# Kernel tuning notes

Measured on AMD Instinct MI355X. Metric: run time of the kernel, lower is better.

Reference implementation:

```python
import jax, jax.numpy as jnp
import numpy as np

B, T, V, D, H = 256, 64, 6207, 512, 512  # batch, seq_len, vocab, emb_dim, hidden_dim
YF = 2048   # image feature dim -> concat with h (512) = 2560 gate input
EPS = 1e-10


def setup_inputs() -> dict:
    key = jax.random.key(0)
    ks = jax.random.split(key, 20)
    # torch init_parameters(): all params ~ U(-0.05, 0.05)
    u = lambda k, s: jax.random.uniform(k, s, jnp.float32, -0.05, 0.05)
    return {
        "y": jax.random.normal(ks[0], (B, YF), jnp.float32),
        "x": jax.random.randint(ks[1], (B, T), 0, V),
        "emb_w": u(ks[2], (V, D)),
        # bottom LSTM cell (input 512 -> hidden 512), torch layout: W_ih (4H, D)
        "W_ih": u(ks[3], (4 * H, D)), "W_hh": u(ks[4], (4 * H, H)),
        "b_ih": u(ks[5], (4 * H,)), "b_hh": u(ks[6], (4 * H,)),
        # top LSTM cell (input 512 -> hidden 512)
        "W_ih_t": u(ks[7], (4 * H, H)), "W_hh_t": u(ks[8], (4 * H, H)),
        "b_ih_t": u(ks[9], (4 * H,)), "b_hh_t": u(ks[10], (4 * H,)),
        # gate linear: Linear(2560, 512)
        "Wg": u(ks[11], (H, H + YF)), "bg": u(ks[12], (H,)),
        # final linear: Linear(512, 256)
        "Wlin": u(ks[13], (256, H)), "blin": u(ks[14], (256,)),
        # per-step gumbel-sigmoid uniforms (sampled inside forward in torch;
        # precomputed here so the reference is deterministic)
        "u1": jax.random.uniform(ks[15], (T, B, H), jnp.float32),
        "u2": jax.random.uniform(ks[16], (T, B, H), jnp.float32),
    }


def _lstm_cell(xt, h, c, Wi, Wh, bi, bh):
    # torch nn.LSTM gate order: i, f, g, o
    z = xt @ Wi.T + bi + h @ Wh.T + bh          # (B, 4H)
    i, f, g, o = jnp.split(z, 4, axis=-1)
    c = jax.nn.sigmoid(f) * c + jax.nn.sigmoid(i) * jnp.tanh(g)
    h = jax.nn.sigmoid(o) * jnp.tanh(c)
    return h, c


def reference(y, x, emb_w, W_ih, W_hh, b_ih, b_hh,
              W_ih_t, W_hh_t, b_ih_t, b_hh_t, Wg, bg, Wlin, blin, u1, u2):
    xs = jnp.transpose(emb_w[x], (1, 0, 2))     # (T, B, D)

    def step(carry, ins):
        h, c, ht, ct = carry
        xt, u1t, u2t = ins
        h, c = _lstm_cell(xt, h, c, W_ih, W_hh, b_ih, b_hh)
        # gate logits: relu(Linear([h, y]))
        logits = jax.nn.relu(jnp.concatenate([h, y], axis=1) @ Wg.T + bg)
        # custom gumbel-sigmoid noise: -log(log(U2+eps)/log(U1+eps)+eps)
        noise = -jnp.log(jnp.log(u2t + EPS) / jnp.log(u1t + EPS) + EPS)
        y_soft = jax.nn.sigmoid(logits + noise)
        # hard threshold at 0.5 with straight-through estimator
        y_hard = (y_soft >= 0.5).astype(y_soft.dtype)
        gate = y_hard - jax.lax.stop_gradient(y_soft) + y_soft
        hf = h * gate
        ht, ct = _lstm_cell(hf, ht, ct, W_ih_t, W_hh_t, b_ih_t, b_hh_t)
        return (h, c, ht, ct), None

    z0 = jnp.zeros((B, H), jnp.float32)
    (_, _, ht, _), _ = jax.lax.scan(step, (z0, z0, z0, z0), (xs, u1, u2))
    # dropout is identity in eval mode; torch output is (1, B, 256), squeezed here
    return jax.nn.relu(ht @ Wlin.T + blin)      # (B, 256)
```

## Files before the change

### kernel.cpp

```cpp
#include <hip/hip_runtime.h>
#include <hip/hip_bf16.h>


typedef __attribute__((ext_vector_type(8))) short short8;
typedef __attribute__((ext_vector_type(4))) float floatx4;

#define MFMA16(a, b, c) __builtin_amdgcn_mfma_f32_16x16x32_bf16(a, b, c, 0, 0, 0)
#define AGENT __HIP_MEMORY_SCOPE_AGENT
#define HWREG_XCC_ID ((31u << 11) | (0u << 6) | 20u)

__device__ inline float bf2f(ushort u) {
    union { unsigned int u32; float f; } v; v.u32 = ((unsigned int)u) << 16; return v.f;
}
__device__ inline ushort f2bf(float f) {
    union { float f; unsigned int u; } v; v.f = f;
    return (ushort)((v.u + 0x7fffu + ((v.u >> 16) & 1u)) >> 16);
}
__device__ inline short8 ld8(const ushort* p) { return *(const short8*)p; }
__device__ inline float sigf(float x) { return 1.0f / (1.0f + expf(-x)); }
__device__ inline void mm3(floatx4& acc, short8 ah, short8 al, short8 bh, short8 bl) {
    acc = MFMA16(ah, bh, acc);
    acc = MFMA16(ah, bl, acc);
    acc = MFMA16(al, bh, acc);
}

__global__ __launch_bounds__(256) void k_prep(const float* __restrict__ w0,
                                              const float* __restrict__ w1,
                                              const float* __restrict__ w2,
                                              const float* __restrict__ w3,
                                              const float* __restrict__ wg,
                                              const float* __restrict__ wl,
                                              const float* __restrict__ em,
                                              const float* __restrict__ yy,
                                              ushort* __restrict__ wreg,
                                              uint* __restrict__ zbase) {
    unsigned i = blockIdx.x * 256u + threadIdx.x;
    if (i >= 9735712u) return;
    if (i >= 9338368u) {
        zbase[i - 9338368u] = 0u;
        return;
    }
    const float* src; ushort* hi; unsigned n, loc;
    if (i < 4194304u) {
        unsigned seg = i >> 20; loc = i & 1048575u; n = 1048576u;
        hi = wreg + seg * 2097152u;
        src = (seg == 0) ? w0 : (seg == 1) ? w1 : (seg == 2) ? w2 : w3;
    } else if (i < 5505024u) { loc = i - 4194304u; src = wg; hi = wreg + 8388608u;  n = 1310720u; }
    else if (i < 5636096u)   { loc = i - 5505024u; src = wl; hi = wreg + 11010048u; n = 131072u; }
    else if (i < 8814080u)   { loc = i - 5636096u; src = em; hi = wreg + 11272192u; n = 3177984u; }
    else                     { loc = i - 8814080u; src = yy; hi = wreg + 17628160u; n = 524288u; }
    float v = src[loc];
    ushort h = f2bf(v);
    hi[loc] = h;
    hi[n + loc] = f2bf(v - bf2f(h));
}

__global__ __launch_bounds__(512) void k_gy(const ushort* __restrict__ y_hi,
                                            const ushort* __restrict__ y_lo,
                                            const ushort* __restrict__ Wg_hi,
                                            const ushort* __restrict__ Wg_lo,
                                            const float* __restrict__ bg,
                                            float* __restrict__ gy) {
    __shared__ float zsB[4 * 528];
    int tid = threadIdx.x, lane = tid & 63, w = tid >> 6;
    int quad = lane >> 4, lr = lane & 15, q8 = quad * 8;
    int r0 = (blockIdx.x >> 4) * 16, n0 = (blockIdx.x & 15) * 32;
    int nh = w & 1, kq = w >> 1;
    int arow = r0 + lr, brow = n0 + nh * 16 + lr;
    floatx4 acc = {};
#pragma unroll
    for (int k0 = 0; k0 < 512; k0 += 32) {
        short8 ah = ld8(y_hi + arow * 2048 + kq * 512 + k0 + q8);
        short8 al = ld8(y_lo + arow * 2048 + kq * 512 + k0 + q8);
        short8 bh = ld8(Wg_hi + brow * 2560 + 512 + kq * 512 + k0 + q8);
        short8 bl = ld8(Wg_lo + brow * 2560 + 512 + kq * 512 + k0 + q8);
        mm3(acc, ah, al, bh, bl);
    }
#pragma unroll
    for (int r4 = 0; r4 < 4; r4++)
        zsB[kq * 528 + (quad * 4 + r4) * 33 + nh * 16 + lr] = acc[r4];
    __syncthreads();
    int ml = tid >> 5, jj = tid & 31;
    float s = zsB[ml * 33 + jj] + zsB[528 + ml * 33 + jj] +
              zsB[1056 + ml * 33 + jj] + zsB[1584 + ml * 33 + jj];
    gy[(r0 + ml) * 512 + n0 + jj] = s + bg[n0 + jj];
}

struct KP {
    const float *b_ih, *b_hh, *b_iht, *b_hht, *u1, *u2, *gy;
    const int* x;
    uint* gflags;
    uint* claim;
    uint *hP, *htP0, *htP1, *hfP;
    ushort *ht_hi, *ht_lo;
    const ushort *Whh_hi, *Whh_lo, *Wih_hi, *Wih_lo;
    const ushort *Wiht_hi, *Wiht_lo, *Whht_hi, *Whht_lo;
    const ushort *Wg_hi, *Wg_lo, *em_hi, *em_lo;
};

__device__ inline void gbar_arrive(uint* gf, int jb, uint g) {
    __builtin_amdgcn_s_waitcnt(0);
    asm volatile("" ::: "memory");
    __syncthreads();
    if (threadIdx.x == 0)
        __hip_atomic_store(&gf[jb], g, __ATOMIC_RELAXED, AGENT);
}
__device__ inline void gbar_wait(const uint* gf, uint g) {
    if ((threadIdx.x >> 6) == 0) {
        int l = threadIdx.x & 63;
        for (;;) {
            uint v = (l < 16) ? __hip_atomic_load(&gf[l], __ATOMIC_RELAXED, AGENT) : g;
            if (__all((int)(v >= g))) break;
            __builtin_amdgcn_s_sleep(1);
        }
    }
    __syncthreads();
}

__device__ inline void stage_state(const uint* __restrict__ src, int r0,
                                   ushort* __restrict__ dst) {
    int tid = threadIdx.x;
    int sr = tid >> 5, scol = (tid & 31) * 16;
    const unsigned long long* p =
        (const unsigned long long*)(src + (r0 + sr) * 512 + scol);
    ushort* d = dst + sr * 1032;
#pragma unroll
    for (int i = 0; i < 8; i++) {
        unsigned long long v = __hip_atomic_load(p + i, __ATOMIC_RELAXED, AGENT);
        uint u0 = (uint)v, u1v = (uint)(v >> 32);
        int c = scol + i * 2;
        *(uint*)(d + c) = (u0 & 0xffffu) | ((u1v & 0xffffu) << 16);
        *(uint*)(d + 520 + c) = (u0 >> 16) | (u1v & 0xffff0000u);
    }
}

__device__ inline void stage_emb(const ushort* __restrict__ emh,
                                 const ushort* __restrict__ eml,
                                 const int* __restrict__ x, int r0, int t,
                                 ushort* __restrict__ dst) {
    int tid = threadIdx.x;
    int sr = tid >> 5, sc = (tid & 31) * 16;
    int tok = x[(r0 + sr) * 64 + t];
    const short8* ph = (const short8*)(emh + (size_t)tok * 512 + sc);
    const short8* pl = (const short8*)(eml + (size_t)tok * 512 + sc);
    short8 h0 = ph[0], h1 = ph[1], l0 = pl[0], l1 = pl[1];
    ushort* d = dst + sr * 1032;
    *(short8*)(d + sc) = h0;       *(short8*)(d + sc + 8) = h1;
    *(short8*)(d + 520 + sc) = l0; *(short8*)(d + 520 + sc + 8) = l1;
}

__device__ inline short8 fragA(const ushort* As, int row, int k) {
    return *(const short8*)(As + row * 1032 + k);
}

__global__ void __launch_bounds__(512, 1) k_main(KP p) {
    __shared__ ushort As[16 * 1032];
    __shared__ ushort Ae[16 * 1032];
    __shared__ ushort Az[16 * 1032];
    __shared__ ushort Ac[16 * 1032];
    __shared__ float zs[16 * 132];
    __shared__ uint role_s;

    const int tid = threadIdx.x;
    const int w = tid >> 6;
    const int lane = tid & 63;
    const int quad = lane >> 4;
    const int lr = lane & 15;
    const int q8 = quad * 8;
    const float EPS = 1e-10f;

    if (tid == 0) {
        uint xcc = __builtin_amdgcn_s_getreg(HWREG_XCC_ID) & 7u;
        uint slot = __hip_atomic_fetch_add(&p.claim[xcc * 16], 1u,
                                           __ATOMIC_RELAXED, AGENT) & 31u;
        role_s = xcc * 32u + slot;
    }
    __syncthreads();
    const uint role = role_s;
    const int jb = (int)(role >> 4);
    const int g16 = (int)(role & 15u);
    const int r0 = g16 * 16, j0 = jb * 32;

    const int gate = w >> 1, nh = w & 1;
    const int brow = gate * 512 + j0 + nh * 16 + lr;
    const int kq = w >> 1;
    const int browB = j0 + nh * 16 + lr;
    const int ml = tid >> 5, jj = tid & 31;

    const float biasA = p.b_ih[brow] + p.b_hh[brow];
    const float biasC = p.b_iht[brow] + p.b_hht[brow];
    const float gy_r = p.gy[(r0 + ml) * 512 + j0 + jj];
    const ushort* WhhH = p.Whh_hi + brow * 512;
    const ushort* WhhL = p.Whh_lo + brow * 512;
    const ushort* WihH = p.Wih_hi + brow * 512;
    const ushort* WihL = p.Wih_lo + brow * 512;
    const ushort* WitH = p.Wiht_hi + brow * 512;
    const ushort* WitL = p.Wiht_lo + brow * 512;
    const ushort* WhtH = p.Whht_hi + brow * 512;
    const ushort* WhtL = p.Whht_lo + brow * 512;
    const ushort* WgH = p.Wg_hi + browB * 2560 + kq * 128;
    const ushort* WgL = p.Wg_lo + browB * 2560 + kq * 128;
    const float* pu1 = p.u1 + (r0 + ml) * 512 + j0 + jj;
    const float* pu2 = p.u2 + (r0 + ml) * 512 + j0 + jj;
    uint* gf = p.gflags + g16 * 16;

    for (int i = tid; i < 16 * 1032; i += 512) As[i] = 0;
    stage_emb(p.em_hi, p.em_lo, p.x, r0, 0, Ae);
    __syncthreads();

    float c_reg = 0.0f, ct_reg = 0.0f;
    uint g = 0;

    for (int t = 0; t < 64; t++) {
        {
            floatx4 a1 = {}, a2 = {};
#pragma unroll
            for (int k0 = 0; k0 < 512; k0 += 32) {
                mm3(a1, fragA(As, lr, k0 + q8), fragA(As, lr, 520 + k0 + q8),
                    ld8(WhhH + k0 + q8), ld8(WhhL + k0 + q8));
                mm3(a2, fragA(Ae, lr, k0 + q8), fragA(Ae, lr, 520 + k0 + q8),
                    ld8(WihH + k0 + q8), ld8(WihL + k0 + q8));
            }
#pragma unroll
            for (int r4 = 0; r4 < 4; r4++)
                zs[(quad * 4 + r4) * 132 + gate * 32 + nh * 16 + lr] =
                    a1[r4] + a2[r4] + biasA;
        }
        __syncthreads();
        {
            float zi = zs[ml * 132 + jj],      zf = zs[ml * 132 + 32 + jj];
            float zg = zs[ml * 132 + 64 + jj], zo = zs[ml * 132 + 96 + jj];
            c_reg = sigf(zf) * c_reg + sigf(zi) * tanhf(zg);
            float hv = sigf(zo) * tanhf(c_reg);
            ushort hb = f2bf(hv);
            ushort lb = f2bf(hv - bf2f(hb));
            __hip_atomic_store(&p.hP[(r0 + ml) * 512 + j0 + jj],
                               (uint)hb | ((uint)lb << 16), __ATOMIC_RELAXED, AGENT);
        }
        g++;
        gbar_arrive(gf, jb, g);
        float U1 = __builtin_nontemporal_load(pu1 + t * 131072);
        float U2 = __builtin_nontemporal_load(pu2 + t * 131072);
        float noise = -logf(logf(U2 + EPS) / logf(U1 + EPS) + EPS);
        gbar_wait(gf, g);

        stage_state(p.hP, r0, As);
        __syncthreads();
        {
            floatx4 acc = {};
#pragma unroll
            for (int k0 = 0; k0 < 128; k0 += 32)
                mm3(acc, fragA(As, lr, kq * 128 + k0 + q8),
                    fragA(As, lr, 520 + kq * 128 + k0 + q8),
                    ld8(WgH + k0 + q8), ld8(WgL + k0 + q8));
#pragma unroll
            for (int r4 = 0; r4 < 4; r4++)
                zs[kq * 528 + (quad * 4 + r4) * 33 + nh * 16 + lr] = acc[r4];
        }
        __syncthreads();
        {
            float z2 = zs[ml * 33 + jj] + zs[528 + ml * 33 + jj] +
                       zs[1056 + ml * 33 + jj] + zs[1584 + ml * 33 + jj];
            float logit = fmaxf(z2 + gy_r, 0.0f);
            bool gbit = sigf(logit + noise) >= 0.5f;
            ushort hb = As[ml * 1032 + j0 + jj];
            ushort lb = As[ml * 1032 + 520 + j0 + jj];
            uint pk = gbit ? ((uint)hb | ((uint)lb << 16)) : 0u;
            __hip_atomic_store(&p.hfP[(r0 + ml) * 512 + j0 + jj], pk,
                               __ATOMIC_RELAXED, AGENT);
        }
        g++;
        gbar_arrive(gf, jb, g);
        stage_state((t & 1) ? p.htP0 : p.htP1, r0, Az);
        if (t < 63) stage_emb(p.em_hi, p.em_lo, p.x, r0, t + 1, Ae);
        gbar_wait(gf, g);

        stage_state(p.hfP, r0, Ac);
        __syncthreads();
        {
            floatx4 c1 = {}, c2 = {};
#pragma unroll
            for (int k0 = 0; k0 < 512; k0 += 32) {
                mm3(c1, fragA(Ac, lr, k0 + q8), fragA(Ac, lr, 520 + k0 + q8),
                    ld8(WitH + k0 + q8), ld8(WitL + k0 + q8));
                mm3(c2, fragA(Az, lr, k0 + q8), fragA(Az, lr, 520 + k0 + q8),
                    ld8(WhtH + k0 + q8), ld8(WhtL + k0 + q8));
            }
#pragma unroll
            for (int r4 = 0; r4 < 4; r4++)
                zs[(quad * 4 + r4) * 132 + gate * 32 + nh * 16 + lr] =
                    c1[r4] + c2[r4] + biasC;
        }
        __syncthreads();
        {
            float zi = zs[ml * 132 + jj],      zf = zs[ml * 132 + 32 + jj];
            float zg = zs[ml * 132 + 64 + jj], zo = zs[ml * 132 + 96 + jj];
            ct_reg = sigf(zf) * ct_reg + sigf(zi) * tanhf(zg);
            float hv = sigf(zo) * tanhf(ct_reg);
            ushort hb = f2bf(hv);
            ushort lb = f2bf(hv - bf2f(hb));
            int idx = (r0 + ml) * 512 + j0 + jj;
            uint* htcur = (t & 1) ? p.htP1 : p.htP0;
            __hip_atomic_store(&htcur[idx], (uint)hb | ((uint)lb << 16),
                               __ATOMIC_RELAXED, AGENT);
            if (t == 63) { p.ht_hi[idx] = hb; p.ht_lo[idx] = lb; }
        }
        __syncthreads();
    }
}

__global__ __launch_bounds__(256) void k_final(const ushort* __restrict__ ht_hi,
                                               const ushort* __restrict__ ht_lo,
                                               const ushort* __restrict__ Wl_hi,
                                               const ushort* __restrict__ Wl_lo,
                                               const float* __restrict__ blin,
                                               float* __restrict__ out) {
    int tid = threadIdx.x, lane = tid & 63, w = tid >> 6;
    int wm = w & 1, wn = w >> 1, quad = lane >> 4, lr = lane & 15;
    int m0 = blockIdx.y * 64, n0 = blockIdx.x * 64;
    floatx4 acc[2][2] = {};
    for (int k0 = 0; k0 < 512; k0 += 32) {
        short8 ah[2], al[2], bh[2], bl[2];
#pragma unroll
        for (int tn = 0; tn < 2; tn++) {
            int n = n0 + wn * 32 + tn * 16 + lr;
            bh[tn] = ld8(Wl_hi + n * 512 + k0 + quad * 8);
            bl[tn] = ld8(Wl_lo + n * 512 + k0 + quad * 8);
        }
#pragma unroll
        for (int tm = 0; tm < 2; tm++) {
            int r = m0 + wm * 32 + tm * 16 + lr;
            ah[tm] = ld8(ht_hi + r * 512 + k0 + quad * 8);
            al[tm] = ld8(ht_lo + r * 512 + k0 + quad * 8);
        }
#pragma unroll
        for (int tm = 0; tm < 2; tm++)
#pragma unroll
            for (int tn = 0; tn < 2; tn++) mm3(acc[tm][tn], ah[tm], al[tm], bh[tn], bl[tn]);
    }
#pragma unroll
    for (int tm = 0; tm < 2; tm++)
#pragma unroll
        for (int tn = 0; tn < 2; tn++)
#pragma unroll
            for (int r4 = 0; r4 < 4; r4++) {
                int row = m0 + wm * 32 + tm * 16 + quad * 4 + r4;
                int n = n0 + wn * 32 + tn * 16 + lr;
                out[row * 256 + n] = fmaxf(acc[tm][tn][r4] + blin[n], 0.0f);
            }
}

extern "C" void kernel_launch(void* const* d_in, const int* in_sizes, int n_in,
                              void* d_out, int out_size, void* d_ws, size_t ws_size,
                              hipStream_t stream) {
    (void)in_sizes; (void)n_in; (void)out_size; (void)ws_size;
    const float* y      = (const float*)d_in[0];
    const int*   x      = (const int*)d_in[1];
    const float* emb    = (const float*)d_in[2];
    const float* W_ih   = (const float*)d_in[3];
    const float* W_hh   = (const float*)d_in[4];
    const float* b_ih   = (const float*)d_in[5];
    const float* b_hh   = (const float*)d_in[6];
    const float* W_iht  = (const float*)d_in[7];
    const float* W_hht  = (const float*)d_in[8];
    const float* b_iht  = (const float*)d_in[9];
    const float* b_hht  = (const float*)d_in[10];
    const float* Wg     = (const float*)d_in[11];
    const float* bg     = (const float*)d_in[12];
    const float* Wlin   = (const float*)d_in[13];
    const float* blin   = (const float*)d_in[14];
    const float* u1     = (const float*)d_in[15];
    const float* u2     = (const float*)d_in[16];
    float* out = (float*)d_out;

    uint* bar = (uint*)d_ws;
    uint* hP   = bar + 4128;
    uint* htP0 = hP + 131072;
    uint* htP1 = htP0 + 131072;
    uint* hfP  = htP1 + 131072;
    float* gy  = (float*)(hfP + 131072);
    ushort* ht_hi = (ushort*)(gy + 131072);
    ushort* ht_lo = ht_hi + 131072;
    ushort* wreg  = ht_lo + 131072;

    KP p;
    p.b_ih = b_ih; p.b_hh = b_hh; p.b_iht = b_iht; p.b_hht = b_hht;
    p.u1 = u1; p.u2 = u2; p.gy = gy; p.x = x;
    p.gflags = bar; p.claim = bar + 1024;
    p.hP = hP; p.htP0 = htP0; p.htP1 = htP1; p.hfP = hfP;
    p.ht_hi = ht_hi; p.ht_lo = ht_lo;
    p.Wih_hi  = wreg;             p.Wih_lo  = wreg + 1048576;
    p.Whh_hi  = wreg + 2097152;   p.Whh_lo  = wreg + 3145728;
    p.Wiht_hi = wreg + 4194304;   p.Wiht_lo = wreg + 5242880;
    p.Whht_hi = wreg + 6291456;   p.Whht_lo = wreg + 7340032;
    p.Wg_hi   = wreg + 8388608;   p.Wg_lo   = wreg + 9699328;
    p.em_hi   = wreg + 11272192;  p.em_lo   = wreg + 14450176;
    const ushort* Wl_hi = wreg + 11010048; const ushort* Wl_lo = wreg + 11141120;
    const ushort* y_hi  = wreg + 17628160; const ushort* y_lo  = wreg + 18152448;

    k_prep<<<dim3(38030), dim3(256), 0, stream>>>(W_ih, W_hh, W_iht, W_hht, Wg, Wlin,
                                                  emb, y, wreg, bar);
    k_gy<<<dim3(256), dim3(512), 0, stream>>>(y_hi, y_lo, p.Wg_hi, p.Wg_lo, bg, gy);

    void* args[] = {(void*)&p};
    hipLaunchCooperativeKernel((const void*)k_main, dim3(256), dim3(512), args, 0, stream);

    k_final<<<dim3(4, 4), dim3(256), 0, stream>>>(ht_hi, ht_lo, Wl_hi, Wl_lo, blin, out);
}
```

Before: 2.809 ms.

## Exchange gate bits instead of gated hidden state, overlap top-LSTM recurrent matmul with barrier

The second inter-block exchange per step now sends a ballot-packed bitmask of gate decisions rather than full hf values. Each block rebuilds the gated hidden state locally from its staged h. The Whh_t recurrent matmul is split around the bit-barrier poll so half of it overlaps the wait. h is double-buffered so stages can proceed without an extra barrier, and state loads use batched sc0/sc1 dwordx4 loads issued together before unpacking. This cuts exchanged data and hides sync latency, at the cost of more LDS work and reliance on cache-bypass semantics for correctness.

```diff
diff --git a/kernel.cpp b/kernel.cpp
--- a/kernel.cpp
+++ b/kernel.cpp
@@ -4,6 +4,7 @@
 
 typedef __attribute__((ext_vector_type(8))) short short8;
 typedef __attribute__((ext_vector_type(4))) float floatx4;
+typedef __attribute__((ext_vector_type(4))) unsigned int uintx4;
 
 #define MFMA16(a, b, c) __builtin_amdgcn_mfma_f32_16x16x32_bf16(a, b, c, 0, 0, 0)
 #define AGENT __HIP_MEMORY_SCOPE_AGENT
@@ -35,7 +36,7 @@
                                               ushort* __restrict__ wreg,
                                               uint* __restrict__ zbase) {
     unsigned i = blockIdx.x * 256u + threadIdx.x;
-    if (i >= 9735712u) return;
+    if (i >= 9866784u) return;
     if (i >= 9338368u) {
         zbase[i - 9338368u] = 0u;
         return;
@@ -89,48 +90,59 @@
 struct KP {
     const float *b_ih, *b_hh, *b_iht, *b_hht, *u1, *u2, *gy;
     const int* x;
-    uint* gflags;
+    uint *hseq, *bseq;
     uint* claim;
-    uint *hP, *htP0, *htP1, *hfP;
+    uint *hP0, *hP1, *htP0, *htP1, *bitsP;
     ushort *ht_hi, *ht_lo;
     const ushort *Whh_hi, *Whh_lo, *Wih_hi, *Wih_lo;
     const ushort *Wiht_hi, *Wiht_lo, *Whht_hi, *Whht_lo;
     const ushort *Wg_hi, *Wg_lo, *em_hi, *em_lo;
 };
 
-__device__ inline void gbar_arrive(uint* gf, int jb, uint g) {
+__device__ inline void publish(uint* sq, uint v) {
+    asm volatile("" ::: "memory");
     __builtin_amdgcn_s_waitcnt(0);
-    asm volatile("" ::: "memory");
     __syncthreads();
     if (threadIdx.x == 0)
-        __hip_atomic_store(&gf[jb], g, __ATOMIC_RELAXED, AGENT);
-}
-__device__ inline void gbar_wait(const uint* gf, uint g) {
+        __hip_atomic_store(sq, v, __ATOMIC_RELAXED, AGENT);
+}
+__device__ inline void poll16(const uint* sq, uint target) {
     if ((threadIdx.x >> 6) == 0) {
         int l = threadIdx.x & 63;
         for (;;) {
-            uint v = (l < 16) ? __hip_atomic_load(&gf[l], __ATOMIC_RELAXED, AGENT) : g;
-            if (__all((int)(v >= g))) break;
+            uint v = (l < 16) ? __hip_atomic_load(&sq[l], __ATOMIC_RELAXED, AGENT) : target;
+            if (__all((int)(v >= target))) break;
             __builtin_amdgcn_s_sleep(1);
         }
     }
     __syncthreads();
 }
 
-__device__ inline void stage_state(const uint* __restrict__ src, int r0,
-                                   ushort* __restrict__ dst) {
+__device__ inline void issue_row16(const uint* __restrict__ src, int r0, uintx4* v) {
     int tid = threadIdx.x;
     int sr = tid >> 5, scol = (tid & 31) * 16;
-    const unsigned long long* p =
-        (const unsigned long long*)(src + (r0 + sr) * 512 + scol);
+    const uint* pp = src + (r0 + sr) * 512 + scol;
+    asm volatile(
+        "global_load_dwordx4 %0, %4, off sc0 sc1\n\t"
+        "global_load_dwordx4 %1, %4, off offset:16 sc0 sc1\n\t"
+        "global_load_dwordx4 %2, %4, off offset:32 sc0 sc1\n\t"
+        "global_load_dwordx4 %3, %4, off offset:48 sc0 sc1"
+        : "=v"(v[0]), "=v"(v[1]), "=v"(v[2]), "=v"(v[3])
+        : "v"(pp) : "memory");
+}
+__device__ inline void unpack_row16(const uintx4* v, ushort* __restrict__ dst) {
+    int tid = threadIdx.x;
+    int sr = tid >> 5, scol = (tid & 31) * 16;
     ushort* d = dst + sr * 1032;
 #pragma unroll
-    for (int i = 0; i < 8; i++) {
-        unsigned long long v = __hip_atomic_load(p + i, __ATOMIC_RELAXED, AGENT);
-        uint u0 = (uint)v, u1v = (uint)(v >> 32);
-        int c = scol + i * 2;
-        *(uint*)(d + c) = (u0 & 0xffffu) | ((u1v & 0xffffu) << 16);
-        *(uint*)(d + 520 + c) = (u0 >> 16) | (u1v & 0xffff0000u);
+    for (int i = 0; i < 4; i++) {
+#pragma unroll
+        for (int jp = 0; jp < 2; jp++) {
+            uint u0 = v[i][jp * 2], u1v = v[i][jp * 2 + 1];
+            int c = scol + i * 4 + jp * 2;
+            *(uint*)(d + c) = (u0 & 0xffffu) | ((u1v & 0xffffu) << 16);
+            *(uint*)(d + 520 + c) = (u0 >> 16) | (u1v & 0xffff0000u);
+        }
     }
 }
 
@@ -159,6 +171,7 @@
     __shared__ ushort Az[16 * 1032];
     __shared__ ushort Ac[16 * 1032];
     __shared__ float zs[16 * 132];
+    __shared__ uint gbits[256];
     __shared__ uint role_s;
 
     const int tid = threadIdx.x;
@@ -202,14 +215,14 @@
     const ushort* WgL = p.Wg_lo + browB * 2560 + kq * 128;
     const float* pu1 = p.u1 + (r0 + ml) * 512 + j0 + jj;
     const float* pu2 = p.u2 + (r0 + ml) * 512 + j0 + jj;
-    uint* gf = p.gflags + g16 * 16;
+    uint* hs = p.hseq + g16 * 16;
+    uint* bs = p.bseq + g16 * 16;
 
     for (int i = tid; i < 16 * 1032; i += 512) As[i] = 0;
     stage_emb(p.em_hi, p.em_lo, p.x, r0, 0, Ae);
     __syncthreads();
 
     float c_reg = 0.0f, ct_reg = 0.0f;
-    uint g = 0;
 
     for (int t = 0; t < 64; t++) {
         {
@@ -227,6 +240,7 @@
                     a1[r4] + a2[r4] + biasA;
         }
         __syncthreads();
+        uint* hPcur = (t & 1) ? p.hP1 : p.hP0;
         {
             float zi = zs[ml * 132 + jj],      zf = zs[ml * 132 + 32 + jj];
             float zg = zs[ml * 132 + 64 + jj], zo = zs[ml * 132 + 96 + jj];
@@ -234,18 +248,24 @@
             float hv = sigf(zo) * tanhf(c_reg);
             ushort hb = f2bf(hv);
             ushort lb = f2bf(hv - bf2f(hb));
-            __hip_atomic_store(&p.hP[(r0 + ml) * 512 + j0 + jj],
+            __hip_atomic_store(&hPcur[(r0 + ml) * 512 + j0 + jj],
                                (uint)hb | ((uint)lb << 16), __ATOMIC_RELAXED, AGENT);
         }
-        g++;
-        gbar_arrive(gf, jb, g);
+        publish(&hs[jb], (uint)(t + 1));
         float U1 = __builtin_nontemporal_load(pu1 + t * 131072);
         float U2 = __builtin_nontemporal_load(pu2 + t * 131072);
         float noise = -logf(logf(U2 + EPS) / logf(U1 + EPS) + EPS);
-        gbar_wait(gf, g);
-
-        stage_state(p.hP, r0, As);
-        __syncthreads();
+        poll16(hs, (uint)(t + 1));
+        uintx4 va[4], vz[4];
+        issue_row16(hPcur, r0, va);
+        issue_row16((t & 1) ? p.htP0 : p.htP1, r0, vz);
+        if (t < 63) stage_emb(p.em_hi, p.em_lo, p.x, r0, t + 1, Ae);
+        asm volatile("s_waitcnt vmcnt(0)" ::: "memory");
+        __builtin_amdgcn_sched_barrier(0);
+        unpack_row16(va, As);
+        unpack_row16(vz, Az);
+        __syncthreads();
+
         {
             floatx4 acc = {};
 #pragma unroll
@@ -263,33 +283,56 @@
                        zs[1056 + ml * 33 + jj] + zs[1584 + ml * 33 + jj];
             float logit = fmaxf(z2 + gy_r, 0.0f);
             bool gbit = sigf(logit + noise) >= 0.5f;
-            ushort hb = As[ml * 1032 + j0 + jj];
-            ushort lb = As[ml * 1032 + 520 + j0 + jj];
-            uint pk = gbit ? ((uint)hb | ((uint)lb << 16)) : 0u;
-            __hip_atomic_store(&p.hfP[(r0 + ml) * 512 + j0 + jj], pk,
-                               __ATOMIC_RELAXED, AGENT);
-        }
-        g++;
-        gbar_arrive(gf, jb, g);
-        stage_state((t & 1) ? p.htP0 : p.htP1, r0, Az);
-        if (t < 63) stage_emb(p.em_hi, p.em_lo, p.x, r0, t + 1, Ae);
-        gbar_wait(gf, g);
-
-        stage_state(p.hfP, r0, Ac);
-        __syncthreads();
-        {
-            floatx4 c1 = {}, c2 = {};
-#pragma unroll
-            for (int k0 = 0; k0 < 512; k0 += 32) {
-                mm3(c1, fragA(Ac, lr, k0 + q8), fragA(Ac, lr, 520 + k0 + q8),
+            unsigned long long bm = __ballot((int)gbit);
+            if ((lane & 31) == 0)
+                __hip_atomic_store(&p.bitsP[(r0 + ml) * 16 + jb],
+                                   (uint)(bm >> ((lane >> 5) * 32)),
+                                   __ATOMIC_RELAXED, AGENT);
+        }
+        publish(&bs[jb], (uint)(t + 1));
+
+        floatx4 c2a = {};
+#pragma unroll
+        for (int k0 = 0; k0 < 256; k0 += 32)
+            mm3(c2a, fragA(Az, lr, k0 + q8), fragA(Az, lr, 520 + k0 + q8),
+                ld8(WhtH + k0 + q8), ld8(WhtL + k0 + q8));
+        poll16(bs, (uint)(t + 1));
+        uint rb = 0;
+        if (tid < 256)
+            asm volatile("global_load_dword %0, %1, off sc0 sc1"
+                         : "=v"(rb) : "v"(p.bitsP + r0 * 16 + tid) : "memory");
+#pragma unroll
+        for (int k0 = 256; k0 < 512; k0 += 32)
+            mm3(c2a, fragA(Az, lr, k0 + q8), fragA(Az, lr, 520 + k0 + q8),
+                ld8(WhtH + k0 + q8), ld8(WhtL + k0 + q8));
+        asm volatile("s_waitcnt vmcnt(0)" ::: "memory");
+        __builtin_amdgcn_sched_barrier(0);
+        if (tid < 256) gbits[tid] = rb;
+        __syncthreads();
+        {
+            int sr = tid >> 5, sc = (tid & 31) * 16;
+            uint word = gbits[sr * 16 + (sc >> 5)];
+            uint chunk = (word >> (sc & 16)) & 0xffffu;
+            const ushort* as0 = As + sr * 1032 + sc;
+            ushort* ac0 = Ac + sr * 1032 + sc;
+#pragma unroll
+            for (int j = 0; j < 16; j++) {
+                ushort m = (ushort)(0u - ((chunk >> j) & 1u));
+                ac0[j] = (ushort)(as0[j] & m);
+                ac0[520 + j] = (ushort)(as0[520 + j] & m);
+            }
+        }
+        __syncthreads();
+        {
+            floatx4 c1a = {};
+#pragma unroll
+            for (int k0 = 0; k0 < 512; k0 += 32)
+                mm3(c1a, fragA(Ac, lr, k0 + q8), fragA(Ac, lr, 520 + k0 + q8),
                     ld8(WitH + k0 + q8), ld8(WitL + k0 + q8));
-                mm3(c2, fragA(Az, lr, k0 + q8), fragA(Az, lr, 520 + k0 + q8),
-                    ld8(WhtH + k0 + q8), ld8(WhtL + k0 + q8));
-            }
 #pragma unroll
             for (int r4 = 0; r4 < 4; r4++)
                 zs[(quad * 4 + r4) * 132 + gate * 32 + nh * 16 + lr] =
-                    c1[r4] + c2[r4] + biasC;
+                    c1a[r4] + c2a[r4] + biasC;
         }
         __syncthreads();
         {
@@ -373,21 +416,22 @@
     const float* u2     = (const float*)d_in[16];
     float* out = (float*)d_out;
 
-    uint* bar = (uint*)d_ws;
-    uint* hP   = bar + 4128;
-    uint* htP0 = hP + 131072;
+    uint* bar  = (uint*)d_ws;
+    uint* hP0  = bar + 4128;
+    uint* hP1  = hP0 + 131072;
+    uint* htP0 = hP1 + 131072;
     uint* htP1 = htP0 + 131072;
-    uint* hfP  = htP1 + 131072;
-    float* gy  = (float*)(hfP + 131072);
+    float* gy  = (float*)(htP1 + 131072);
     ushort* ht_hi = (ushort*)(gy + 131072);
     ushort* ht_lo = ht_hi + 131072;
-    ushort* wreg  = ht_lo + 131072;
+    uint* bitsP = (uint*)(ht_lo + 131072);
+    ushort* wreg = (ushort*)(bitsP + 4096);
 
     KP p;
     p.b_ih = b_ih; p.b_hh = b_hh; p.b_iht = b_iht; p.b_hht = b_hht;
     p.u1 = u1; p.u2 = u2; p.gy = gy; p.x = x;
-    p.gflags = bar; p.claim = bar + 1024;
-    p.hP = hP; p.htP0 = htP0; p.htP1 = htP1; p.hfP = hfP;
+    p.hseq = bar; p.bseq = bar + 256; p.claim = bar + 1024;
+    p.hP0 = hP0; p.hP1 = hP1; p.htP0 = htP0; p.htP1 = htP1; p.bitsP = bitsP;
     p.ht_hi = ht_hi; p.ht_lo = ht_lo;
     p.Wih_hi  = wreg;             p.Wih_lo  = wreg + 1048576;
     p.Whh_hi  = wreg + 2097152;   p.Whh_lo  = wreg + 3145728;
@@ -398,7 +442,7 @@
     const ushort* Wl_hi = wreg + 11010048; const ushort* Wl_lo = wreg + 11141120;
     const ushort* y_hi  = wreg + 17628160; const ushort* y_lo  = wreg + 18152448;
 
-    k_prep<<<dim3(38030), dim3(256), 0, stream>>>(W_ih, W_hh, W_iht, W_hht, Wg, Wlin,
+    k_prep<<<dim3(38543), dim3(256), 0, stream>>>(W_ih, W_hh, W_iht, W_hht, Wg, Wlin,
                                                   emb, y, wreg, bar);
     k_gy<<<dim3(256), dim3(512), 0, stream>>>(y_hi, y_lo, p.Wg_hi, p.Wg_lo, bg, gy);
 
```

New measurement: 2.725 ms. -3.0%, faster.
